# Kernel optimization log

Measured on AMD Instinct MI355X. Metric: run time of the kernel, lower is better.

## Reference

```python
import jax, jax.numpy as jnp
import numpy as np

ALPHA = 0.2  # LeakyReLU negative slope
IN_FEATURES = 512
OUT_FEATURES = 512
N_NODES = 8192


def setup_inputs() -> dict:
    key = jax.random.key(0)
    k1, k2, k3, k4 = jax.random.split(key, 4)
    nodes = jax.random.normal(k1, (N_NODES, IN_FEATURES), dtype=jnp.float32)
    adj = jax.random.uniform(k2, (N_NODES, N_NODES), dtype=jnp.float32)
    # Parameters (torch nn.Linear layout: [out, in])
    W = jax.random.normal(k3, (OUT_FEATURES, IN_FEATURES), dtype=jnp.float32) * (1.0 / np.sqrt(IN_FEATURES))
    a = jax.random.normal(k4, (2 * OUT_FEATURES,), dtype=jnp.float32) * (1.0 / np.sqrt(2 * OUT_FEATURES))
    return {"nodes": nodes, "adj": adj, "W": W, "a": a}


def reference(nodes, adj, W, a):
    # h = W(nodes): [N, F_out]
    h = nodes @ W.T
    f_out = h.shape[1]
    # Decompose a([h_i || h_j]) = h_i @ a1 + h_j @ a2 -- avoids the O(N^2 * 2F)
    # concatenated tensor of the naive implementation; same math.
    s1 = h @ a[:f_out]   # [N] contribution of row node i
    s2 = h @ a[f_out:]   # [N] contribution of col node j
    e = jax.nn.leaky_relu(s1[:, None] + s2[None, :], negative_slope=ALPHA)  # [N, N]
    e = jnp.where(adj >= 0.5, e, -jnp.inf)  # mask non-edges (adj < 0.5)
    attention = jax.nn.softmax(e, axis=1)
    # dropout omitted: reference corresponds to eval mode (training=False)
    return attention
```

## Files before the change

kernel.cpp:

```cpp
#include <hip/hip_runtime.h>
#include <math.h>

#define N_NODES 8192
#define F_IN    512
#define F_OUT   512
#define ALPHA   0.2f

__global__ void k_wpart(const float* __restrict__ W, const float* __restrict__ a,
                        float* __restrict__ p1, float* __restrict__ p2) {
    const int b = blockIdx.x;
    const int t = threadIdx.x;
    const int k1 = t, k2 = t + 256;
    float a1k1 = 0.f, a1k2 = 0.f, a2k1 = 0.f, a2k2 = 0.f;
#pragma unroll
    for (int oo = 0; oo < 16; ++oo) {
        const int o = b * 16 + oo;
        const float a1 = a[o];
        const float a2 = a[F_OUT + o];
        const float w1 = W[(size_t)o * F_IN + k1];
        const float w2 = W[(size_t)o * F_IN + k2];
        a1k1 += w1 * a1;  a1k2 += w2 * a1;
        a2k1 += w1 * a2;  a2k2 += w2 * a2;
    }
    p1[b * 512 + k1] = a1k1;  p1[b * 512 + k2] = a1k2;
    p2[b * 512 + k1] = a2k1;  p2[b * 512 + k2] = a2k2;
}

__global__ void k_vreduce(const float* __restrict__ p1, const float* __restrict__ p2,
                          float* __restrict__ v1, float* __restrict__ v2) {
    const int k = blockIdx.x * 256 + threadIdx.x;
    float s1 = 0.f, s2 = 0.f;
#pragma unroll
    for (int b = 0; b < 32; ++b) {
        s1 += p1[b * 512 + k];
        s2 += p2[b * 512 + k];
    }
    v1[k] = s1;
    v2[k] = s2;
}

__global__ void k_scores(const float* __restrict__ nodes,
                         const float* __restrict__ v1, const float* __restrict__ v2,
                         float* __restrict__ s1, float* __restrict__ s2) {
    const int wave = threadIdx.x >> 6;
    const int lane = threadIdx.x & 63;
    const int row  = blockIdx.x * 4 + wave;
    const float4* np4 = (const float4*)(nodes + (size_t)row * F_IN);
    const float4* v14 = (const float4*)v1;
    const float4* v24 = (const float4*)v2;
    float acc1 = 0.f, acc2 = 0.f;
#pragma unroll
    for (int i = 0; i < 2; ++i) {
        const int idx = i * 64 + lane;
        const float4 n  = np4[idx];
        const float4 w1 = v14[idx];
        const float4 w2 = v24[idx];
        acc1 += n.x * w1.x + n.y * w1.y + n.z * w1.z + n.w * w1.w;
        acc2 += n.x * w2.x + n.y * w2.y + n.z * w2.z + n.w * w2.w;
    }
#pragma unroll
    for (int off = 32; off; off >>= 1) {
        acc1 += __shfl_xor(acc1, off);
        acc2 += __shfl_xor(acc2, off);
    }
    if (lane == 0) {
        s1[row] = acc1;
        s2[row] = acc2;
    }
}

__global__ void __launch_bounds__(256)
k_softmax(const float* __restrict__ adj, const float* __restrict__ s1g,
          const float* __restrict__ s2g, float* __restrict__ out) {
    const int row = blockIdx.x;
    const int tid = threadIdx.x;
    const int wave = tid >> 6;
    const int lane = tid & 63;
    const size_t rowoff = (size_t)row * N_NODES;
    const float s1i = s1g[row];

    const float4* adj4 = (const float4*)(adj + rowoff);
    const float4* s24  = (const float4*)s2g;
    float4* out4 = (float4*)(out + rowoff);

    __shared__ float redmax[4];
    __shared__ float redsum[4];

    float4 t[8];
    float vmax = -INFINITY;

#pragma unroll
    for (int it = 0; it < 8; ++it) {
        const int j4 = it * 256 + tid;
        const float4 av = adj4[j4];
        const float4 sv = s24[j4];
        float4 e;
        {
            float x = s1i + sv.x; x = fmaxf(x, ALPHA * x);
            e.x = (av.x >= 0.5f) ? x : -INFINITY;
        }
        {
            float x = s1i + sv.y; x = fmaxf(x, ALPHA * x);
            e.y = (av.y >= 0.5f) ? x : -INFINITY;
        }
        {
            float x = s1i + sv.z; x = fmaxf(x, ALPHA * x);
            e.z = (av.z >= 0.5f) ? x : -INFINITY;
        }
        {
            float x = s1i + sv.w; x = fmaxf(x, ALPHA * x);
            e.w = (av.w >= 0.5f) ? x : -INFINITY;
        }
        vmax = fmaxf(vmax, fmaxf(fmaxf(e.x, e.y), fmaxf(e.z, e.w)));
        t[it] = e;
    }

#pragma unroll
    for (int off = 32; off; off >>= 1)
        vmax = fmaxf(vmax, __shfl_xor(vmax, off));
    if (lane == 0) redmax[wave] = vmax;
    __syncthreads();
    const float m = fmaxf(fmaxf(redmax[0], redmax[1]), fmaxf(redmax[2], redmax[3]));

    float sum = 0.f;
#pragma unroll
    for (int it = 0; it < 8; ++it) {
        float4 e = t[it];
        e.x = __expf(e.x - m);
        e.y = __expf(e.y - m);
        e.z = __expf(e.z - m);
        e.w = __expf(e.w - m);
        sum += (e.x + e.y) + (e.z + e.w);
        t[it] = e;
    }
#pragma unroll
    for (int off = 32; off; off >>= 1)
        sum += __shfl_xor(sum, off);
    if (lane == 0) redsum[wave] = sum;
    __syncthreads();
    const float total = (redsum[0] + redsum[1]) + (redsum[2] + redsum[3]);
    const float inv = 1.0f / total;

#pragma unroll
    for (int it = 0; it < 8; ++it) {
        const int j4 = it * 256 + tid;
        float4 e = t[it];
        e.x *= inv; e.y *= inv; e.z *= inv; e.w *= inv;
        out4[j4] = e;
    }
}

extern "C" void kernel_launch(void* const* d_in, const int* in_sizes, int n_in,
                              void* d_out, int out_size, void* d_ws, size_t ws_size,
                              hipStream_t stream) {
    const float* nodes = (const float*)d_in[0];
    const float* adj   = (const float*)d_in[1];
    const float* W     = (const float*)d_in[2];
    const float* a     = (const float*)d_in[3];
    float* out = (float*)d_out;

    float* ws = (float*)d_ws;
    float* v1 = ws;
    float* v2 = ws + 512;
    float* s1 = ws + 1024;
    float* s2 = ws + 1024 + 8192;
    float* p1 = ws + 1024 + 16384;
    float* p2 = p1 + 32 * 512;

    k_wpart  <<<32,   256, 0, stream>>>(W, a, p1, p2);
    k_vreduce<<<2,    256, 0, stream>>>(p1, p2, v1, v2);
    k_scores <<<2048, 256, 0, stream>>>(nodes, v1, v2, s1, s2);
    k_softmax<<<8192, 256, 0, stream>>>(adj, s1, s2, out);
}
```

Before: 453.1 us.

## Use nontemporal loads/stores, 512-thread blocks, and single-pass online softmax merge

Softmax rows now use 512 threads with 4 float4 per thread, and load adj and store out with nontemporal hints to avoid cache pollution. Each thread computes a local max and exp-sum, and these are merged across lanes and waves with an online-softmax combine. This removes one block barrier and the separate max pass before exp. It adds extra exp calls in the merge and a possible NaN edge when a whole wave is masked.

```diff
diff --git a/kernel.cpp b/kernel.cpp
--- a/kernel.cpp
+++ b/kernel.cpp
@@ -5,6 +5,8 @@
 #define F_IN    512
 #define F_OUT   512
 #define ALPHA   0.2f
+
+typedef float f32x4 __attribute__((ext_vector_type(4)));
 
 __global__ void k_wpart(const float* __restrict__ W, const float* __restrict__ a,
                         float* __restrict__ p1, float* __restrict__ p2) {
@@ -69,84 +71,82 @@
     }
 }
 
-__global__ void __launch_bounds__(256)
+__global__ void __launch_bounds__(512)
 k_softmax(const float* __restrict__ adj, const float* __restrict__ s1g,
           const float* __restrict__ s2g, float* __restrict__ out) {
-    const int row = blockIdx.x;
-    const int tid = threadIdx.x;
+    const int row  = blockIdx.x;
+    const int tid  = threadIdx.x;
     const int wave = tid >> 6;
     const int lane = tid & 63;
     const size_t rowoff = (size_t)row * N_NODES;
     const float s1i = s1g[row];
 
-    const float4* adj4 = (const float4*)(adj + rowoff);
-    const float4* s24  = (const float4*)s2g;
-    float4* out4 = (float4*)(out + rowoff);
+    const f32x4* adj4 = (const f32x4*)(adj + rowoff);
+    const float4* s24 = (const float4*)s2g;
+    f32x4* out4 = (f32x4*)(out + rowoff);
 
-    __shared__ float redmax[4];
-    __shared__ float redsum[4];
+    __shared__ float redm[8];
+    __shared__ float redl[8];
 
-    float4 t[8];
-    float vmax = -INFINITY;
+    f32x4 u[4];
+    float mt = -INFINITY;
 
 #pragma unroll
-    for (int it = 0; it < 8; ++it) {
-        const int j4 = it * 256 + tid;
-        const float4 av = adj4[j4];
+    for (int it = 0; it < 4; ++it) {
+        const int j4 = it * 512 + tid;
+        const f32x4 av = __builtin_nontemporal_load(&adj4[j4]);
         const float4 sv = s24[j4];
-        float4 e;
-        {
-            float x = s1i + sv.x; x = fmaxf(x, ALPHA * x);
-            e.x = (av.x >= 0.5f) ? x : -INFINITY;
-        }
-        {
-            float x = s1i + sv.y; x = fmaxf(x, ALPHA * x);
-            e.y = (av.y >= 0.5f) ? x : -INFINITY;
-        }
-        {
-            float x = s1i + sv.z; x = fmaxf(x, ALPHA * x);
-            e.z = (av.z >= 0.5f) ? x : -INFINITY;
-        }
-        {
-            float x = s1i + sv.w; x = fmaxf(x, ALPHA * x);
-            e.w = (av.w >= 0.5f) ? x : -INFINITY;
-        }
-        vmax = fmaxf(vmax, fmaxf(fmaxf(e.x, e.y), fmaxf(e.z, e.w)));
-        t[it] = e;
+        f32x4 e;
+        { float x = s1i + sv.x; x = fmaxf(x, ALPHA * x); e.x = (av.x >= 0.5f) ? x : -INFINITY; }
+        { float x = s1i + sv.y; x = fmaxf(x, ALPHA * x); e.y = (av.y >= 0.5f) ? x : -INFINITY; }
+        { float x = s1i + sv.z; x = fmaxf(x, ALPHA * x); e.z = (av.z >= 0.5f) ? x : -INFINITY; }
+        { float x = s1i + sv.w; x = fmaxf(x, ALPHA * x); e.w = (av.w >= 0.5f) ? x : -INFINITY; }
+        mt = fmaxf(mt, fmaxf(fmaxf(e.x, e.y), fmaxf(e.z, e.w)));
+        u[it] = e;
     }
 
+    const float msafe = (mt == -INFINITY) ? 0.f : mt;
+
+    float lt = 0.f;
 #pragma unroll
-    for (int off = 32; off; off >>= 1)
-        vmax = fmaxf(vmax, __shfl_xor(vmax, off));
-    if (lane == 0) redmax[wave] = vmax;
+    for (int it = 0; it < 4; ++it) {
+        f32x4 e = u[it];
+        e.x = __expf(e.x - msafe);
+        e.y = __expf(e.y - msafe);
+        e.z = __expf(e.z - msafe);
+        e.w = __expf(e.w - msafe);
+        lt += (e.x + e.y) + (e.z + e.w);
+        u[it] = e;
+    }
+
+    float m = mt, l = lt;
+#pragma unroll
+    for (int off = 32; off; off >>= 1) {
+        const float mo = __shfl_xor(m, off);
+        const float lo = __shfl_xor(l, off);
+        const float M  = fmaxf(m, mo);
+        l = l * __expf(m - M) + lo * __expf(mo - M);
+        m = M;
+    }
+    if (lane == 0) { redm[wave] = m; redl[wave] = l; }
     __syncthreads();
-    const float m = fmaxf(fmaxf(redmax[0], redmax[1]), fmaxf(redmax[2], redmax[3]));
-
-    float sum = 0.f;
+    float M = redm[0], L = redl[0];
 #pragma unroll
-    for (int it = 0; it < 8; ++it) {
-        float4 e = t[it];
-        e.x = __expf(e.x - m);
-        e.y = __expf(e.y - m);
-        e.z = __expf(e.z - m);
-        e.w = __expf(e.w - m);
-        sum += (e.x + e.y) + (e.z + e.w);
-        t[it] = e;
+    for (int w = 1; w < 8; ++w) {
+        const float mo = redm[w];
+        const float lo = redl[w];
+        const float Mn = fmaxf(M, mo);
+        L = L * __expf(M - Mn) + lo * __expf(mo - Mn);
+        M = Mn;
     }
-#pragma unroll
-    for (int off = 32; off; off >>= 1)
-        sum += __shfl_xor(sum, off);
-    if (lane == 0) redsum[wave] = sum;
-    __syncthreads();
-    const float total = (redsum[0] + redsum[1]) + (redsum[2] + redsum[3]);
-    const float inv = 1.0f / total;
+    const float scale = __expf(msafe - M) / L;
 
 #pragma unroll
-    for (int it = 0; it < 8; ++it) {
-        const int j4 = it * 256 + tid;
-        float4 e = t[it];
-        e.x *= inv; e.y *= inv; e.z *= inv; e.w *= inv;
-        out4[j4] = e;
+    for (int it = 0; it < 4; ++it) {
+        const int j4 = it * 512 + tid;
+        f32x4 e = u[it];
+        e.x *= scale; e.y *= scale; e.z *= scale; e.w *= scale;
+        __builtin_nontemporal_store(e, &out4[j4]);
     }
 }
 
@@ -170,5 +170,5 @@
     k_wpart  <<<32,   256, 0, stream>>>(W, a, p1, p2);
     k_vreduce<<<2,    256, 0, stream>>>(p1, p2, v1, v2);
     k_scores <<<2048, 256, 0, stream>>>(nodes, v1, v2, s1, s2);
-    k_softmax<<<8192, 256, 0, stream>>>(adj, s1, s2, out);
+    k_softmax<<<8192, 512, 0, stream>>>(adj, s1, s2, out);
 }
```

After: 444.7 us. Within noise of the previous version (-1.9%).
